# Kernel optimization log

Hardware: AMD Instinct MI355X
Metric: run time of the kernel (lower is better)

Reference implementation:

```python
import jax, jax.numpy as jnp
import numpy as np

N, C, K = 100000, 64, 27
EPS = 1e-5


def setup_inputs() -> dict:
    key = jax.random.key(0)
    ks = jax.random.split(key, 8)
    feats = jax.random.normal(ks[0], (N, C), dtype=jnp.float32)
    W1 = jax.random.normal(ks[1], (K, C, C), dtype=jnp.float32) * (1.0 / np.sqrt(K * C))
    W2 = jax.random.normal(ks[2], (K, C, C), dtype=jnp.float32) * (1.0 / np.sqrt(K * C))
    gamma1 = jnp.ones((C,), dtype=jnp.float32)
    beta1 = jnp.zeros((C,), dtype=jnp.float32)
    gamma2 = jnp.ones((C,), dtype=jnp.float32)
    beta2 = jnp.zeros((C,), dtype=jnp.float32)
    nbr_idx1 = jax.random.randint(ks[3], (K, N), 0, N, dtype=jnp.int32)
    nbr_idx2 = jax.random.randint(ks[4], (K, N), 0, N, dtype=jnp.int32)
    nbr_mask1 = (jax.random.uniform(ks[5], (K, N)) < 0.7).astype(jnp.float32)
    nbr_mask2 = (jax.random.uniform(ks[6], (K, N)) < 0.7).astype(jnp.float32)
    return {"feats": feats, "W1": W1, "gamma1": gamma1, "beta1": beta1,
            "W2": W2, "gamma2": gamma2, "beta2": beta2,
            "nbr_idx1": nbr_idx1, "nbr_mask1": nbr_mask1,
            "nbr_idx2": nbr_idx2, "nbr_mask2": nbr_mask2}


def sparse_conv(f, idx, mask, W):
    # gather per kernel offset: [K, N, C], mask out missing neighbors
    g = f[idx] * mask[..., None]
    # per-offset GEMM and accumulate over offsets -> [N, C_out]
    return jnp.einsum('knc,kcd->nd', g, W)


def batch_norm(x, gamma, beta):
    # MinkowskiBatchNorm (training): stats over all N points, per channel
    mean = jnp.mean(x, axis=0)
    var = jnp.mean(jnp.square(x - mean), axis=0)
    return (x - mean) * jax.lax.rsqrt(var + EPS) * gamma + beta


def reference(feats, W1, gamma1, beta1, W2, gamma2, beta2,
              nbr_idx1, nbr_mask1, nbr_idx2, nbr_mask2):
    out = sparse_conv(feats, nbr_idx1, nbr_mask1, W1)
    out = jax.nn.relu(batch_norm(out, gamma1, beta1))
    out = sparse_conv(out, nbr_idx2, nbr_mask2, W2)
    out = batch_norm(out, gamma2, beta2)
    out = out + feats          # identity residual (stride=1, no downsample)
    return jax.nn.relu(out)
```

## Files before the change

kernel.cpp:

```cpp
#include <hip/hip_runtime.h>
#include <hip/hip_bf16.h>
#include <stdint.h>
#include <stddef.h>

#define N_PTS 100000
#define KOFF 27

typedef __attribute__((ext_vector_type(8))) __bf16 bf16x8;
typedef __attribute__((ext_vector_type(4))) float f32x4;

__device__ inline unsigned short f2bf(float f) {
  union { float f; unsigned u; } x; x.f = f;
  unsigned r = x.u + 0x7fffu + ((x.u >> 16) & 1u);
  return (unsigned short)(r >> 16);
}

__global__ __launch_bounds__(256) void prep_kernel(const float* __restrict__ feats,
                                                   const float* __restrict__ W1,
                                                   const float* __restrict__ W2,
                                                   unsigned short* __restrict__ featsb,
                                                   unsigned short* __restrict__ f2b,
                                                   unsigned short* __restrict__ wf1,
                                                   unsigned short* __restrict__ wf2,
                                                   float* __restrict__ stats) {
  __shared__ float sW[4096];
  int t = threadIdx.x;
  if (blockIdx.x < 54) {
    int which = blockIdx.x & 1;
    int k = blockIdx.x >> 1;
    const float* W = (which ? W2 : W1) + (size_t)k * 4096;
    unsigned short* wf = (which ? wf2 : wf1) + (size_t)k * 4096;
#pragma unroll
    for (int i = 0; i < 4; ++i)
      ((float4*)sW)[t + 256 * i] = ((const float4*)W)[t + 256 * i];
    __syncthreads();
#pragma unroll
    for (int i = 0; i < 16; ++i) {
      int o = i * 256 + t;
      int j = o & 7, l = (o >> 3) & 63, nt = (o >> 9) & 3, kk = (o >> 11) & 1;
      int c = kk * 32 + ((l >> 4) << 3) + j;
      int d = nt * 16 + (l & 15);
      wf[o] = f2bf(sW[c * 64 + d]);
    }
    return;
  }
  int fb = blockIdx.x - 54;
  int NB = gridDim.x - 54;
  const int NF4 = N_PTS * 16;
  for (int i = fb * 256 + t; i < NF4; i += NB * 256) {
    float4 v = ((const float4*)feats)[i];
    ushort4 o;
    o.x = f2bf(v.x); o.y = f2bf(v.y); o.z = f2bf(v.z); o.w = f2bf(v.w);
    ((ushort4*)featsb)[i] = o;
  }
  if (fb == 0) {
    if (t < 256) stats[t] = 0.f;
    uint4 z = make_uint4(0u, 0u, 0u, 0u);
    if (t < 8)            ((uint4*)(featsb + (size_t)N_PTS * 64))[t] = z;
    if (t >= 8 && t < 16) ((uint4*)(f2b    + (size_t)N_PTS * 64))[t - 8] = z;
  }
}

#define MFMA16(a, b, c) __builtin_amdgcn_mfma_f32_16x16x32_bf16(__builtin_bit_cast(bf16x8, a), __builtin_bit_cast(bf16x8, b), c, 0, 0, 0)

#define STEP(kcur, Aca0, Acb0, Aca1, Acb1, Ana0, Anb0, Ana1, Anb1,              \
             iN0, mN0, iN1, mN1, iF0, mF0, iF1, mF1)                            \
  {                                                                             \
    const size_t kn = (size_t)((kcur) + 1) * 8192;                              \
    S0 = *(const uint4*)(wfB + kn + t16);                                       \
    S1 = *(const uint4*)(wfB + kn + 4096 + t16);                                \
    {                                                                           \
      int gie = (mN0 != 0.f) ? iN0 : N_PTS;                                     \
      const char* rp = (const char*)fin + (size_t)gie * 128 + g16;              \
      Ana0 = *(const uint4*)rp; Anb0 = *(const uint4*)(rp + 64);                \
    }                                                                           \
    {                                                                           \
      int gie = (mN1 != 0.f) ? iN1 : N_PTS;                                     \
      const char* rp = (const char*)fin + (size_t)gie * 128 + g16;              \
      Ana1 = *(const uint4*)rp; Anb1 = *(const uint4*)(rp + 64);                \
    }                                                                           \
    {                                                                           \
      int kf = ((kcur) + 2 <= 26) ? (kcur) + 2 : 26;                            \
      iF0 = idxp0[(size_t)kf * N_PTS];                                          \
      float mt0 = mp0[(size_t)kf * N_PTS]; mF0 = v0 ? mt0 : 0.f;                \
      iF1 = idxp1[(size_t)kf * N_PTS];                                          \
      float mt1 = mp1[(size_t)kf * N_PTS]; mF1 = v1 ? mt1 : 0.f;                \
    }                                                                           \
    {                                                                           \
      const uint4* bL = (const uint4*)sB[cur];                                  \
      uint4 b0 = bL[lane],       b1 = bL[64 + lane];                            \
      uint4 b2 = bL[128 + lane], b3 = bL[192 + lane];                           \
      uint4 b4 = bL[256 + lane], b5 = bL[320 + lane];                           \
      uint4 b6 = bL[384 + lane], b7 = bL[448 + lane];                           \
      a00 = MFMA16(Aca0, b0, a00); a01 = MFMA16(Aca0, b1, a01);                 \
      a02 = MFMA16(Aca0, b2, a02); a03 = MFMA16(Aca0, b3, a03);                 \
      a10 = MFMA16(Aca1, b0, a10); a11 = MFMA16(Aca1, b1, a11);                 \
      a12 = MFMA16(Aca1, b2, a12); a13 = MFMA16(Aca1, b3, a13);                 \
      a00 = MFMA16(Acb0, b4, a00); a01 = MFMA16(Acb0, b5, a01);                 \
      a02 = MFMA16(Acb0, b6, a02); a03 = MFMA16(Acb0, b7, a03);                 \
      a10 = MFMA16(Acb1, b4, a10); a11 = MFMA16(Acb1, b5, a11);                 \
      a12 = MFMA16(Acb1, b6, a12); a13 = MFMA16(Acb1, b7, a13);                 \
    }                                                                           \
    {                                                                           \
      uint4* wL = (uint4*)sB[cur ^ 1];                                          \
      wL[t] = S0; wL[t + 256] = S1;                                             \
    }                                                                           \
    __syncthreads();                                                            \
    cur ^= 1;                                                                   \
  }

__global__ __launch_bounds__(256, 3) void conv_kernel(
    const unsigned short* __restrict__ fin,
    const unsigned short* __restrict__ wf,
    const int* __restrict__ idx,
    const float* __restrict__ mask,
    float* __restrict__ yout,
    float* __restrict__ gsum,
    float* __restrict__ gsq)
{
  __shared__ __align__(16) unsigned char sB[2][8192];
  __shared__ float s_sum[64], s_sq[64];

  int t    = threadIdx.x;
  int lane = t & 63;
  int wid  = t >> 6;
  int m    = lane & 15;
  int g    = lane >> 4;
  int g16  = g * 16;
  size_t t16 = (size_t)t * 16;
  int nw   = blockIdx.x * 128 + wid * 32;
  int n0r  = nw + m;
  int n1r  = nw + 16 + m;
  bool v0  = n0r < N_PTS;
  bool v1  = n1r < N_PTS;
  int nc0  = v0 ? n0r : 0;
  int nc1  = v1 ? n1r : 0;

  const int*   idxp0 = idx + nc0;
  const int*   idxp1 = idx + nc1;
  const float* mp0   = mask + nc0;
  const float* mp1   = mask + nc1;
  const char*  wfB   = (const char*)wf;

  if (t < 64) { s_sum[t] = 0.f; s_sq[t] = 0.f; }

  f32x4 a00, a01, a02, a03, a10, a11, a12, a13;
#pragma unroll
  for (int r = 0; r < 4; ++r) {
    a00[r] = 0.f; a01[r] = 0.f; a02[r] = 0.f; a03[r] = 0.f;
    a10[r] = 0.f; a11[r] = 0.f; a12[r] = 0.f; a13[r] = 0.f;
  }

  uint4 Aa0, Ab0, Aa1, Ab1;
  uint4 Ba0, Bb0, Ba1, Bb1;
  uint4 S0, S1;
  int iA0, iA1, iB0, iB1;
  float mA0, mA1, mB0, mB1;
  int cur = 0;

  iA0 = idxp0[0]; { float mt = mp0[0]; mA0 = v0 ? mt : 0.f; }
  iA1 = idxp1[0]; { float mt = mp1[0]; mA1 = v1 ? mt : 0.f; }
  S0 = *(const uint4*)(wfB + t16);
  S1 = *(const uint4*)(wfB + 4096 + t16);
  {
    int gie = (mA0 != 0.f) ? iA0 : N_PTS;
    const char* rp = (const char*)fin + (size_t)gie * 128 + g16;
    Aa0 = *(const uint4*)rp; Ab0 = *(const uint4*)(rp + 64);
  }
  {
    int gie = (mA1 != 0.f) ? iA1 : N_PTS;
    const char* rp = (const char*)fin + (size_t)gie * 128 + g16;
    Aa1 = *(const uint4*)rp; Ab1 = *(const uint4*)(rp + 64);
  }
  iB0 = idxp0[N_PTS]; { float mt = mp0[N_PTS]; mB0 = v0 ? mt : 0.f; }
  iB1 = idxp1[N_PTS]; { float mt = mp1[N_PTS]; mB1 = v1 ? mt : 0.f; }
  {
    uint4* wL = (uint4*)sB[0];
    wL[t] = S0; wL[t + 256] = S1;
  }
  __syncthreads();

  for (int kk = 0; kk < 13; ++kk) {
    int k = 2 * kk;
    STEP(k,     Aa0, Ab0, Aa1, Ab1,  Ba0, Bb0, Ba1, Bb1,
         iB0, mB0, iB1, mB1,  iA0, mA0, iA1, mA1);
    STEP(k + 1, Ba0, Bb0, Ba1, Bb1,  Aa0, Ab0, Aa1, Ab1,
         iA0, mA0, iA1, mA1,  iB0, mB0, iB1, mB1);
  }

  {
    const uint4* bL = (const uint4*)sB[cur];
    uint4 b0 = bL[lane],       b1 = bL[64 + lane];
    uint4 b2 = bL[128 + lane], b3 = bL[192 + lane];
    uint4 b4 = bL[256 + lane], b5 = bL[320 + lane];
    uint4 b6 = bL[384 + lane], b7 = bL[448 + lane];
    a00 = MFMA16(Aa0, b0, a00); a01 = MFMA16(Aa0, b1, a01);
    a02 = MFMA16(Aa0, b2, a02); a03 = MFMA16(Aa0, b3, a03);
    a10 = MFMA16(Aa1, b0, a10); a11 = MFMA16(Aa1, b1, a11);
    a12 = MFMA16(Aa1, b2, a12); a13 = MFMA16(Aa1, b3, a13);
    a00 = MFMA16(Ab0, b4, a00); a01 = MFMA16(Ab0, b5, a01);
    a02 = MFMA16(Ab0, b6, a02); a03 = MFMA16(Ab0, b7, a03);
    a10 = MFMA16(Ab1, b4, a10); a11 = MFMA16(Ab1, b5, a11);
    a12 = MFMA16(Ab1, b6, a12); a13 = MFMA16(Ab1, b7, a13);
  }

  float s0 = 0.f, q0 = 0.f, s1 = 0.f, q1 = 0.f;
  float s2 = 0.f, q2 = 0.f, s3 = 0.f, q3 = 0.f;
#pragma unroll
  for (int r = 0; r < 4; ++r) {
    int row0 = nw + g * 4 + r;
    int row1 = nw + 16 + g * 4 + r;
    float u0 = a00[r], u1 = a01[r], u2 = a02[r], u3 = a03[r];
    float w0 = a10[r], w1 = a11[r], w2 = a12[r], w3 = a13[r];
    s0 += u0 + w0; q0 += u0 * u0 + w0 * w0;
    s1 += u1 + w1; q1 += u1 * u1 + w1 * w1;
    s2 += u2 + w2; q2 += u2 * u2 + w2 * w2;
    s3 += u3 + w3; q3 += u3 * u3 + w3 * w3;
    if (row0 < N_PTS) {
      float* yr = yout + (size_t)row0 * 64;
      yr[m] = u0; yr[16 + m] = u1; yr[32 + m] = u2; yr[48 + m] = u3;
    }
    if (row1 < N_PTS) {
      float* yr = yout + (size_t)row1 * 64;
      yr[m] = w0; yr[16 + m] = w1; yr[32 + m] = w2; yr[48 + m] = w3;
    }
  }
  atomicAdd(&s_sum[m],      s0); atomicAdd(&s_sq[m],      q0);
  atomicAdd(&s_sum[16 + m], s1); atomicAdd(&s_sq[16 + m], q1);
  atomicAdd(&s_sum[32 + m], s2); atomicAdd(&s_sq[32 + m], q2);
  atomicAdd(&s_sum[48 + m], s3); atomicAdd(&s_sq[48 + m], q3);
  __syncthreads();
  if (t < 64) {
    atomicAdd(&gsum[t], s_sum[t]);
    atomicAdd(&gsq[t],  s_sq[t]);
  }
}

__global__ void bn1_kernel(const float* __restrict__ y,
                           const float* __restrict__ sum,
                           const float* __restrict__ sq,
                           const float* __restrict__ gamma,
                           const float* __restrict__ beta,
                           unsigned short* __restrict__ outb) {
  __shared__ float s_scale[64], s_shift[64];
  if (threadIdx.x < 64) {
    int c = threadIdx.x;
    float mean = sum[c] * (1.f / N_PTS);
    float var  = sq[c] * (1.f / N_PTS) - mean * mean;
    float inv  = rsqrtf(var + 1e-5f);
    float sc   = gamma[c] * inv;
    s_scale[c] = sc;
    s_shift[c] = beta[c] - mean * sc;
  }
  __syncthreads();
  int tid = blockIdx.x * blockDim.x + threadIdx.x;
  int stride = gridDim.x * blockDim.x;
  const int NT = N_PTS * 16;
  for (int i = tid; i < NT; i += stride) {
    float4 v = ((const float4*)y)[i];
    int c = (i * 4) & 63;
    float r0 = fmaxf(v.x * s_scale[c]     + s_shift[c],     0.f);
    float r1 = fmaxf(v.y * s_scale[c + 1] + s_shift[c + 1], 0.f);
    float r2 = fmaxf(v.z * s_scale[c + 2] + s_shift[c + 2], 0.f);
    float r3 = fmaxf(v.w * s_scale[c + 3] + s_shift[c + 3], 0.f);
    ushort4 o;
    o.x = f2bf(r0); o.y = f2bf(r1); o.z = f2bf(r2); o.w = f2bf(r3);
    ((ushort4*)outb)[i] = o;
  }
}

__global__ void bn2_kernel(const float* __restrict__ y,
                           const float* __restrict__ sum,
                           const float* __restrict__ sq,
                           const float* __restrict__ gamma,
                           const float* __restrict__ beta,
                           const float* __restrict__ feats,
                           float* __restrict__ out) {
  __shared__ float s_scale[64], s_shift[64];
  if (threadIdx.x < 64) {
    int c = threadIdx.x;
    float mean = sum[c] * (1.f / N_PTS);
    float var  = sq[c] * (1.f / N_PTS) - mean * mean;
    float inv  = rsqrtf(var + 1e-5f);
    float sc   = gamma[c] * inv;
    s_scale[c] = sc;
    s_shift[c] = beta[c] - mean * sc;
  }
  __syncthreads();
  int tid = blockIdx.x * blockDim.x + threadIdx.x;
  int stride = gridDim.x * blockDim.x;
  const int NT = N_PTS * 16;
  for (int i = tid; i < NT; i += stride) {
    float4 v = ((const float4*)y)[i];
    float4 f = ((const float4*)feats)[i];
    int c = (i * 4) & 63;
    float4 o;
    o.x = fmaxf(v.x * s_scale[c]     + s_shift[c]     + f.x, 0.f);
    o.y = fmaxf(v.y * s_scale[c + 1] + s_shift[c + 1] + f.y, 0.f);
    o.z = fmaxf(v.z * s_scale[c + 2] + s_shift[c + 2] + f.z, 0.f);
    o.w = fmaxf(v.w * s_scale[c + 3] + s_shift[c + 3] + f.w, 0.f);
    ((float4*)out)[i] = o;
  }
}

extern "C" void kernel_launch(void* const* d_in, const int* in_sizes, int n_in,
                              void* d_out, int out_size, void* d_ws, size_t ws_size,
                              hipStream_t stream) {
  const float* feats  = (const float*)d_in[0];
  const float* W1     = (const float*)d_in[1];
  const float* gamma1 = (const float*)d_in[2];
  const float* beta1  = (const float*)d_in[3];
  const float* W2     = (const float*)d_in[4];
  const float* gamma2 = (const float*)d_in[5];
  const float* beta2  = (const float*)d_in[6];
  const int*   idx1   = (const int*)d_in[7];
  const float* mask1  = (const float*)d_in[8];
  const int*   idx2   = (const int*)d_in[9];
  const float* mask2  = (const float*)d_in[10];
  float* out = (float*)d_out;

  char* ws = (char*)d_ws;
  unsigned short* featsb = (unsigned short*)(ws + 0);
  unsigned short* wf1    = (unsigned short*)(ws + 12800768);
  unsigned short* wf2    = (unsigned short*)(ws + 13021952);
  float*          stats  = (float*)(ws + 13243136);
  unsigned short* f2b    = (unsigned short*)(ws + 13244160);

  float* sum1 = stats;       float* sq1 = stats + 64;
  float* sum2 = stats + 128; float* sq2 = stats + 192;

  float* y = out;

  prep_kernel<<<54 + 640, 256, 0, stream>>>(feats, W1, W2, featsb, f2b, wf1, wf2, stats);

  const int CONV_GRID = (N_PTS + 127) / 128;
  conv_kernel<<<CONV_GRID, 256, 0, stream>>>(featsb, wf1, idx1, mask1, y, sum1, sq1);
  bn1_kernel<<<1024, 256, 0, stream>>>(y, sum1, sq1, gamma1, beta1, f2b);
  conv_kernel<<<CONV_GRID, 256, 0, stream>>>(f2b, wf2, idx2, mask2, y, sum2, sq2);
  bn2_kernel<<<1024, 256, 0, stream>>>(y, sum2, sq2, gamma2, beta2, feats, out);
}
```

Before: 300.6 us.

## Shrink conv tile to 16 rows per wave and store intermediates as bf16

Each conv wave now handles 16 points instead of 32, which halves the accumulator and prefetch registers so occupancy can rise to six blocks per CU, and the grid is doubled. The conv output y is now written as bf16 instead of fp32, and both BN kernels read packed bf16, cutting intermediate traffic roughly in half. Per-wave weight reuse from LDS drops, so weight LDS loads per MFMA double. Rounding the pre-BN activations to bf16 adds precision loss, and the second conv writes its output into the featsb buffer, which is safe only because featsb is dead once the first conv finishes.

```diff
diff --git a/kernel.cpp b/kernel.cpp
--- a/kernel.cpp
+++ b/kernel.cpp
@@ -8,11 +8,16 @@
 
 typedef __attribute__((ext_vector_type(8))) __bf16 bf16x8;
 typedef __attribute__((ext_vector_type(4))) float f32x4;
+typedef __attribute__((ext_vector_type(8))) unsigned short ushort8;
 
 __device__ inline unsigned short f2bf(float f) {
   union { float f; unsigned u; } x; x.f = f;
   unsigned r = x.u + 0x7fffu + ((x.u >> 16) & 1u);
   return (unsigned short)(r >> 16);
+}
+__device__ inline float bf2f(unsigned short b) {
+  union { unsigned u; float f; } x; x.u = ((unsigned)b) << 16;
+  return x.f;
 }
 
 __global__ __launch_bounds__(256) void prep_kernel(const float* __restrict__ feats,
@@ -63,28 +68,20 @@
 
 #define MFMA16(a, b, c) __builtin_amdgcn_mfma_f32_16x16x32_bf16(__builtin_bit_cast(bf16x8, a), __builtin_bit_cast(bf16x8, b), c, 0, 0, 0)
 
-#define STEP(kcur, Aca0, Acb0, Aca1, Acb1, Ana0, Anb0, Ana1, Anb1,              \
-             iN0, mN0, iN1, mN1, iF0, mF0, iF1, mF1)                            \
+#define STEP(kcur, Ac0, Ac1, An0, An1, iN, mN, iF, mF)                          \
   {                                                                             \
     const size_t kn = (size_t)((kcur) + 1) * 8192;                              \
     S0 = *(const uint4*)(wfB + kn + t16);                                       \
     S1 = *(const uint4*)(wfB + kn + 4096 + t16);                                \
     {                                                                           \
-      int gie = (mN0 != 0.f) ? iN0 : N_PTS;                                     \
+      int gie = (mN != 0.f) ? iN : N_PTS;                                       \
       const char* rp = (const char*)fin + (size_t)gie * 128 + g16;              \
-      Ana0 = *(const uint4*)rp; Anb0 = *(const uint4*)(rp + 64);                \
-    }                                                                           \
-    {                                                                           \
-      int gie = (mN1 != 0.f) ? iN1 : N_PTS;                                     \
-      const char* rp = (const char*)fin + (size_t)gie * 128 + g16;              \
-      Ana1 = *(const uint4*)rp; Anb1 = *(const uint4*)(rp + 64);                \
+      An0 = *(const uint4*)rp; An1 = *(const uint4*)(rp + 64);                  \
     }                                                                           \
     {                                                                           \
       int kf = ((kcur) + 2 <= 26) ? (kcur) + 2 : 26;                            \
-      iF0 = idxp0[(size_t)kf * N_PTS];                                          \
-      float mt0 = mp0[(size_t)kf * N_PTS]; mF0 = v0 ? mt0 : 0.f;                \
-      iF1 = idxp1[(size_t)kf * N_PTS];                                          \
-      float mt1 = mp1[(size_t)kf * N_PTS]; mF1 = v1 ? mt1 : 0.f;                \
+      iF = idxp[(size_t)kf * N_PTS];                                            \
+      float mt = mp[(size_t)kf * N_PTS]; mF = valid ? mt : 0.f;                 \
     }                                                                           \
     {                                                                           \
       const uint4* bL = (const uint4*)sB[cur];                                  \
@@ -92,14 +89,10 @@
       uint4 b2 = bL[128 + lane], b3 = bL[192 + lane];                           \
       uint4 b4 = bL[256 + lane], b5 = bL[320 + lane];                           \
       uint4 b6 = bL[384 + lane], b7 = bL[448 + lane];                           \
-      a00 = MFMA16(Aca0, b0, a00); a01 = MFMA16(Aca0, b1, a01);                 \
-      a02 = MFMA16(Aca0, b2, a02); a03 = MFMA16(Aca0, b3, a03);                 \
-      a10 = MFMA16(Aca1, b0, a10); a11 = MFMA16(Aca1, b1, a11);                 \
-      a12 = MFMA16(Aca1, b2, a12); a13 = MFMA16(Aca1, b3, a13);                 \
-      a00 = MFMA16(Acb0, b4, a00); a01 = MFMA16(Acb0, b5, a01);                 \
-      a02 = MFMA16(Acb0, b6, a02); a03 = MFMA16(Acb0, b7, a03);                 \
-      a10 = MFMA16(Acb1, b4, a10); a11 = MFMA16(Acb1, b5, a11);                 \
-      a12 = MFMA16(Acb1, b6, a12); a13 = MFMA16(Acb1, b7, a13);                 \
+      a0 = MFMA16(Ac0, b0, a0); a1 = MFMA16(Ac0, b1, a1);                       \
+      a2 = MFMA16(Ac0, b2, a2); a3 = MFMA16(Ac0, b3, a3);                       \
+      a0 = MFMA16(Ac1, b4, a0); a1 = MFMA16(Ac1, b5, a1);                       \
+      a2 = MFMA16(Ac1, b6, a2); a3 = MFMA16(Ac1, b7, a3);                       \
     }                                                                           \
     {                                                                           \
       uint4* wL = (uint4*)sB[cur ^ 1];                                          \
@@ -109,12 +102,12 @@
     cur ^= 1;                                                                   \
   }
 
-__global__ __launch_bounds__(256, 3) void conv_kernel(
+__global__ __launch_bounds__(256, 6) void conv_kernel(
     const unsigned short* __restrict__ fin,
     const unsigned short* __restrict__ wf,
     const int* __restrict__ idx,
     const float* __restrict__ mask,
-    float* __restrict__ yout,
+    unsigned short* __restrict__ yout,
     float* __restrict__ gsum,
     float* __restrict__ gsq)
 {
@@ -128,52 +121,34 @@
   int g    = lane >> 4;
   int g16  = g * 16;
   size_t t16 = (size_t)t * 16;
-  int nw   = blockIdx.x * 128 + wid * 32;
-  int n0r  = nw + m;
-  int n1r  = nw + 16 + m;
-  bool v0  = n0r < N_PTS;
-  bool v1  = n1r < N_PTS;
-  int nc0  = v0 ? n0r : 0;
-  int nc1  = v1 ? n1r : 0;
-
-  const int*   idxp0 = idx + nc0;
-  const int*   idxp1 = idx + nc1;
-  const float* mp0   = mask + nc0;
-  const float* mp1   = mask + nc1;
-  const char*  wfB   = (const char*)wf;
+  int nw   = blockIdx.x * 64 + wid * 16;
+  int n    = nw + m;
+  bool valid = n < N_PTS;
+  int nc   = valid ? n : 0;
+
+  const int*   idxp = idx + nc;
+  const float* mp   = mask + nc;
+  const char*  wfB  = (const char*)wf;
 
   if (t < 64) { s_sum[t] = 0.f; s_sq[t] = 0.f; }
 
-  f32x4 a00, a01, a02, a03, a10, a11, a12, a13;
-#pragma unroll
-  for (int r = 0; r < 4; ++r) {
-    a00[r] = 0.f; a01[r] = 0.f; a02[r] = 0.f; a03[r] = 0.f;
-    a10[r] = 0.f; a11[r] = 0.f; a12[r] = 0.f; a13[r] = 0.f;
-  }
-
-  uint4 Aa0, Ab0, Aa1, Ab1;
-  uint4 Ba0, Bb0, Ba1, Bb1;
-  uint4 S0, S1;
-  int iA0, iA1, iB0, iB1;
-  float mA0, mA1, mB0, mB1;
+  f32x4 a0, a1, a2, a3;
+#pragma unroll
+  for (int r = 0; r < 4; ++r) { a0[r] = 0.f; a1[r] = 0.f; a2[r] = 0.f; a3[r] = 0.f; }
+
+  uint4 Aa0, Aa1, Ba0, Ba1, S0, S1;
+  int iA, iB; float mA, mB;
   int cur = 0;
 
-  iA0 = idxp0[0]; { float mt = mp0[0]; mA0 = v0 ? mt : 0.f; }
-  iA1 = idxp1[0]; { float mt = mp1[0]; mA1 = v1 ? mt : 0.f; }
+  iA = idxp[0]; { float mt = mp[0]; mA = valid ? mt : 0.f; }
   S0 = *(const uint4*)(wfB + t16);
   S1 = *(const uint4*)(wfB + 4096 + t16);
   {
-    int gie = (mA0 != 0.f) ? iA0 : N_PTS;
+    int gie = (mA != 0.f) ? iA : N_PTS;
     const char* rp = (const char*)fin + (size_t)gie * 128 + g16;
-    Aa0 = *(const uint4*)rp; Ab0 = *(const uint4*)(rp + 64);
-  }
-  {
-    int gie = (mA1 != 0.f) ? iA1 : N_PTS;
-    const char* rp = (const char*)fin + (size_t)gie * 128 + g16;
-    Aa1 = *(const uint4*)rp; Ab1 = *(const uint4*)(rp + 64);
-  }
-  iB0 = idxp0[N_PTS]; { float mt = mp0[N_PTS]; mB0 = v0 ? mt : 0.f; }
-  iB1 = idxp1[N_PTS]; { float mt = mp1[N_PTS]; mB1 = v1 ? mt : 0.f; }
+    Aa0 = *(const uint4*)rp; Aa1 = *(const uint4*)(rp + 64);
+  }
+  iB = idxp[N_PTS]; { float mt = mp[N_PTS]; mB = valid ? mt : 0.f; }
   {
     uint4* wL = (uint4*)sB[0];
     wL[t] = S0; wL[t + 256] = S1;
@@ -182,10 +157,8 @@
 
   for (int kk = 0; kk < 13; ++kk) {
     int k = 2 * kk;
-    STEP(k,     Aa0, Ab0, Aa1, Ab1,  Ba0, Bb0, Ba1, Bb1,
-         iB0, mB0, iB1, mB1,  iA0, mA0, iA1, mA1);
-    STEP(k + 1, Ba0, Bb0, Ba1, Bb1,  Aa0, Ab0, Aa1, Ab1,
-         iA0, mA0, iA1, mA1,  iB0, mB0, iB1, mB1);
+    STEP(k,     Aa0, Aa1,  Ba0, Ba1,  iB, mB,  iA, mA);
+    STEP(k + 1, Ba0, Ba1,  Aa0, Aa1,  iA, mA,  iB, mB);
   }
 
   {
@@ -194,35 +167,27 @@
     uint4 b2 = bL[128 + lane], b3 = bL[192 + lane];
     uint4 b4 = bL[256 + lane], b5 = bL[320 + lane];
     uint4 b6 = bL[384 + lane], b7 = bL[448 + lane];
-    a00 = MFMA16(Aa0, b0, a00); a01 = MFMA16(Aa0, b1, a01);
-    a02 = MFMA16(Aa0, b2, a02); a03 = MFMA16(Aa0, b3, a03);
-    a10 = MFMA16(Aa1, b0, a10); a11 = MFMA16(Aa1, b1, a11);
-    a12 = MFMA16(Aa1, b2, a12); a13 = MFMA16(Aa1, b3, a13);
-    a00 = MFMA16(Ab0, b4, a00); a01 = MFMA16(Ab0, b5, a01);
-    a02 = MFMA16(Ab0, b6, a02); a03 = MFMA16(Ab0, b7, a03);
-    a10 = MFMA16(Ab1, b4, a10); a11 = MFMA16(Ab1, b5, a11);
-    a12 = MFMA16(Ab1, b6, a12); a13 = MFMA16(Ab1, b7, a13);
+    a0 = MFMA16(Aa0, b0, a0); a1 = MFMA16(Aa0, b1, a1);
+    a2 = MFMA16(Aa0, b2, a2); a3 = MFMA16(Aa0, b3, a3);
+    a0 = MFMA16(Aa1, b4, a0); a1 = MFMA16(Aa1, b5, a1);
+    a2 = MFMA16(Aa1, b6, a2); a3 = MFMA16(Aa1, b7, a3);
   }
 
   float s0 = 0.f, q0 = 0.f, s1 = 0.f, q1 = 0.f;
   float s2 = 0.f, q2 = 0.f, s3 = 0.f, q3 = 0.f;
 #pragma unroll
   for (int r = 0; r < 4; ++r) {
-    int row0 = nw + g * 4 + r;
-    int row1 = nw + 16 + g * 4 + r;
-    float u0 = a00[r], u1 = a01[r], u2 = a02[r], u3 = a03[r];
-    float w0 = a10[r], w1 = a11[r], w2 = a12[r], w3 = a13[r];
-    s0 += u0 + w0; q0 += u0 * u0 + w0 * w0;
-    s1 += u1 + w1; q1 += u1 * u1 + w1 * w1;
-    s2 += u2 + w2; q2 += u2 * u2 + w2 * w2;
-    s3 += u3 + w3; q3 += u3 * u3 + w3 * w3;
-    if (row0 < N_PTS) {
-      float* yr = yout + (size_t)row0 * 64;
-      yr[m] = u0; yr[16 + m] = u1; yr[32 + m] = u2; yr[48 + m] = u3;
-    }
-    if (row1 < N_PTS) {
-      float* yr = yout + (size_t)row1 * 64;
-      yr[m] = w0; yr[16 + m] = w1; yr[32 + m] = w2; yr[48 + m] = w3;
+    int row = nw + g * 4 + r;
+    float v0 = a0[r]; s0 += v0; q0 += v0 * v0;
+    float v1 = a1[r]; s1 += v1; q1 += v1 * v1;
+    float v2 = a2[r]; s2 += v2; q2 += v2 * v2;
+    float v3 = a3[r]; s3 += v3; q3 += v3 * v3;
+    if (row < N_PTS) {
+      unsigned short* yr = yout + (size_t)row * 64;
+      yr[m]      = f2bf(v0);
+      yr[16 + m] = f2bf(v1);
+      yr[32 + m] = f2bf(v2);
+      yr[48 + m] = f2bf(v3);
     }
   }
   atomicAdd(&s_sum[m],      s0); atomicAdd(&s_sq[m],      q0);
@@ -236,7 +201,7 @@
   }
 }
 
-__global__ void bn1_kernel(const float* __restrict__ y,
+__global__ void bn1_kernel(const unsigned short* __restrict__ y,
                            const float* __restrict__ sum,
                            const float* __restrict__ sq,
                            const float* __restrict__ gamma,
@@ -255,21 +220,21 @@
   __syncthreads();
   int tid = blockIdx.x * blockDim.x + threadIdx.x;
   int stride = gridDim.x * blockDim.x;
-  const int NT = N_PTS * 16;
+  const int NT = N_PTS * 8;
   for (int i = tid; i < NT; i += stride) {
-    float4 v = ((const float4*)y)[i];
-    int c = (i * 4) & 63;
-    float r0 = fmaxf(v.x * s_scale[c]     + s_shift[c],     0.f);
-    float r1 = fmaxf(v.y * s_scale[c + 1] + s_shift[c + 1], 0.f);
-    float r2 = fmaxf(v.z * s_scale[c + 2] + s_shift[c + 2], 0.f);
-    float r3 = fmaxf(v.w * s_scale[c + 3] + s_shift[c + 3], 0.f);
-    ushort4 o;
-    o.x = f2bf(r0); o.y = f2bf(r1); o.z = f2bf(r2); o.w = f2bf(r3);
-    ((ushort4*)outb)[i] = o;
-  }
-}
-
-__global__ void bn2_kernel(const float* __restrict__ y,
+    ushort8 v = ((const ushort8*)y)[i];
+    int c = (i * 8) & 63;
+    ushort8 o;
+#pragma unroll
+    for (int j = 0; j < 8; ++j) {
+      float f = bf2f(v[j]);
+      o[j] = f2bf(fmaxf(f * s_scale[c + j] + s_shift[c + j], 0.f));
+    }
+    ((ushort8*)outb)[i] = o;
+  }
+}
+
+__global__ void bn2_kernel(const unsigned short* __restrict__ y,
                            const float* __restrict__ sum,
                            const float* __restrict__ sq,
                            const float* __restrict__ gamma,
@@ -289,17 +254,23 @@
   __syncthreads();
   int tid = blockIdx.x * blockDim.x + threadIdx.x;
   int stride = gridDim.x * blockDim.x;
-  const int NT = N_PTS * 16;
+  const int NT = N_PTS * 8;
   for (int i = tid; i < NT; i += stride) {
-    float4 v = ((const float4*)y)[i];
-    float4 f = ((const float4*)feats)[i];
-    int c = (i * 4) & 63;
-    float4 o;
-    o.x = fmaxf(v.x * s_scale[c]     + s_shift[c]     + f.x, 0.f);
-    o.y = fmaxf(v.y * s_scale[c + 1] + s_shift[c + 1] + f.y, 0.f);
-    o.z = fmaxf(v.z * s_scale[c + 2] + s_shift[c + 2] + f.z, 0.f);
-    o.w = fmaxf(v.w * s_scale[c + 3] + s_shift[c + 3] + f.w, 0.f);
-    ((float4*)out)[i] = o;
+    ushort8 v = ((const ushort8*)y)[i];
+    float4 f0 = ((const float4*)feats)[i * 2];
+    float4 f1 = ((const float4*)feats)[i * 2 + 1];
+    int c = (i * 8) & 63;
+    float4 o0, o1;
+    o0.x = fmaxf(bf2f(v[0]) * s_scale[c]     + s_shift[c]     + f0.x, 0.f);
+    o0.y = fmaxf(bf2f(v[1]) * s_scale[c + 1] + s_shift[c + 1] + f0.y, 0.f);
+    o0.z = fmaxf(bf2f(v[2]) * s_scale[c + 2] + s_shift[c + 2] + f0.z, 0.f);
+    o0.w = fmaxf(bf2f(v[3]) * s_scale[c + 3] + s_shift[c + 3] + f0.w, 0.f);
+    o1.x = fmaxf(bf2f(v[4]) * s_scale[c + 4] + s_shift[c + 4] + f1.x, 0.f);
+    o1.y = fmaxf(bf2f(v[5]) * s_scale[c + 5] + s_shift[c + 5] + f1.y, 0.f);
+    o1.z = fmaxf(bf2f(v[6]) * s_scale[c + 6] + s_shift[c + 6] + f1.z, 0.f);
+    o1.w = fmaxf(bf2f(v[7]) * s_scale[c + 7] + s_shift[c + 7] + f1.w, 0.f);
+    ((float4*)out)[i * 2]     = o0;
+    ((float4*)out)[i * 2 + 1] = o1;
   }
 }
 
@@ -329,13 +300,14 @@
   float* sum1 = stats;       float* sq1 = stats + 64;
   float* sum2 = stats + 128; float* sq2 = stats + 192;
 
-  float* y = out;
+  unsigned short* y1 = (unsigned short*)d_out;
+  unsigned short* y2 = featsb;
 
   prep_kernel<<<54 + 640, 256, 0, stream>>>(feats, W1, W2, featsb, f2b, wf1, wf2, stats);
 
-  const int CONV_GRID = (N_PTS + 127) / 128;
-  conv_kernel<<<CONV_GRID, 256, 0, stream>>>(featsb, wf1, idx1, mask1, y, sum1, sq1);
-  bn1_kernel<<<1024, 256, 0, stream>>>(y, sum1, sq1, gamma1, beta1, f2b);
-  conv_kernel<<<CONV_GRID, 256, 0, stream>>>(f2b, wf2, idx2, mask2, y, sum2, sq2);
-  bn2_kernel<<<1024, 256, 0, stream>>>(y, sum2, sq2, gamma2, beta2, feats, out);
-}
+  const int CONV_GRID = (N_PTS + 63) / 64;
+  conv_kernel<<<CONV_GRID, 256, 0, stream>>>(featsb, wf1, idx1, mask1, y1, sum1, sq1);
+  bn1_kernel<<<1024, 256, 0, stream>>>(y1, sum1, sq1, gamma1, beta1, f2b);
+  conv_kernel<<<CONV_GRID, 256, 0, stream>>>(f2b, wf2, idx2, mask2, y2, sum2, sq2);
+  bn2_kernel<<<1024, 256, 0, stream>>>(y2, sum2, sq2, gamma2, beta2, feats, out);
+}
```

Result: slower. 310.3 us (+3.2%).
